# Kernel optimization log

Measured on AMD Instinct MI355X. Metric: run time of the kernel, lower is better.

Reference implementation:

```python
import jax, jax.numpy as jnp
import numpy as np

B, N = 4096, 2048


def setup_inputs() -> dict:
    key = jax.random.key(0)
    k1, k2, k3, k4 = jax.random.split(key, 4)
    return {
        "src_pts3d": jax.random.normal(k1, (B, N, 3), dtype=jnp.float32),
        "tgt_pts3d": jax.random.normal(k2, (B, N, 3), dtype=jnp.float32),
        "kpt_src_mask": jax.random.uniform(k3, (B, N), dtype=jnp.float32),
        "kpt_tgt_mask": jax.random.uniform(k4, (B, N), dtype=jnp.float32),
    }


def reference(src_pts3d, tgt_pts3d, kpt_src_mask, kpt_tgt_mask):
    # H = src^T @ diag(mask_tgt) @ tgt, fused as a masked row-scale contraction: [B,3,3]
    H = jnp.einsum('bnc,bn,bnd->bcd', src_pts3d, kpt_tgt_mask, tgt_pts3d)
    # torch.svd returns V (H = U S V^T); jnp returns Vh, so V = Vh^T
    u, s, vh = jnp.linalg.svd(H)
    v = jnp.swapaxes(vh, -1, -2)              # [B,3,3]
    ut = jnp.swapaxes(u, -1, -2)              # [B,3,3]
    r = v @ ut
    det = jnp.linalg.det(r)                   # [B]
    # branch-free reflection fix: negate 3rd column of V when det(r) < 0
    sign = jnp.where(det < 0, -1.0, 1.0)
    col_scale = jnp.stack([jnp.ones_like(sign), jnp.ones_like(sign), sign], axis=-1)  # [B,3]
    R = (v * col_scale[:, None, :]) @ ut
    return R
```

## Files before the change

### kernel.cpp

```cpp
#include <hip/hip_runtime.h>
#include <math.h>

#define BATCH 4096
#define NPTS  2048
#define THREADS 256

#define ACC(sx, sy, sz, tx, ty, tz, mm) do {                                   \
    float d0 = (mm) * (tx), d1 = (mm) * (ty), d2 = (mm) * (tz);                \
    h[0] = fmaf((sx), d0, h[0]); h[1] = fmaf((sx), d1, h[1]); h[2] = fmaf((sx), d2, h[2]); \
    h[3] = fmaf((sy), d0, h[3]); h[4] = fmaf((sy), d1, h[4]); h[5] = fmaf((sy), d2, h[5]); \
    h[6] = fmaf((sz), d0, h[6]); h[7] = fmaf((sz), d1, h[7]); h[8] = fmaf((sz), d2, h[8]); \
} while (0)

__global__ __launch_bounds__(THREADS)
void reduce_kernel(const float* __restrict__ src, const float* __restrict__ tgt,
                   const float* __restrict__ mask, float* __restrict__ Hout)
{
    const int b = blockIdx.x;
    const float4* s4 = (const float4*)(src  + (size_t)b * (NPTS * 3));
    const float4* t4 = (const float4*)(tgt  + (size_t)b * (NPTS * 3));
    const float4* m4 = (const float4*)(mask + (size_t)b * NPTS);

    float h[9] = {0.f, 0.f, 0.f, 0.f, 0.f, 0.f, 0.f, 0.f, 0.f};

    for (int g = threadIdx.x; g < NPTS / 4; g += THREADS) {
        float4 m  = m4[g];
        float4 sa = s4[3 * g + 0], sb = s4[3 * g + 1], sc = s4[3 * g + 2];
        float4 ta = t4[3 * g + 0], tb = t4[3 * g + 1], tc = t4[3 * g + 2];
        ACC(sa.x, sa.y, sa.z, ta.x, ta.y, ta.z, m.x);
        ACC(sa.w, sb.x, sb.y, ta.w, tb.x, tb.y, m.y);
        ACC(sb.z, sb.w, sc.x, tb.z, tb.w, tc.x, m.z);
        ACC(sc.y, sc.z, sc.w, tc.y, tc.z, tc.w, m.w);
    }

#pragma unroll
    for (int off = 32; off > 0; off >>= 1) {
#pragma unroll
        for (int i = 0; i < 9; ++i) h[i] += __shfl_down(h[i], off);
    }

    __shared__ float sh[THREADS / 64][9];
    const int wid  = threadIdx.x >> 6;
    const int lane = threadIdx.x & 63;
    if (lane == 0) {
#pragma unroll
        for (int i = 0; i < 9; ++i) sh[wid][i] = h[i];
    }
    __syncthreads();

    if (threadIdx.x < 9) {
        const int i = threadIdx.x;
        Hout[(size_t)b * 9 + i] = sh[0][i] + sh[1][i] + sh[2][i] + sh[3][i];
    }
}

__global__ __launch_bounds__(THREADS)
void solve_kernel(const float* __restrict__ Hin, float* __restrict__ out)
{
    const int b = blockIdx.x * THREADS + threadIdx.x;
    if (b >= BATCH) return;

    double H[3][3];
#pragma unroll
    for (int i = 0; i < 9; ++i)
        H[i / 3][i % 3] = (double)Hin[(size_t)b * 9 + i];

    double A[3][3];
#pragma unroll
    for (int i = 0; i < 3; ++i)
#pragma unroll
        for (int j = 0; j < 3; ++j)
            A[i][j] = H[0][i] * H[0][j] + H[1][i] * H[1][j] + H[2][i] * H[2][j];

    double V[3][3] = {{1, 0, 0}, {0, 1, 0}, {0, 0, 1}};

    const int pq[3][3] = {{0, 1, 2}, {0, 2, 1}, {1, 2, 0}};
    for (int sweep = 0; sweep < 6; ++sweep) {
        for (int r = 0; r < 3; ++r) {
            const int p = pq[r][0], q = pq[r][1], k = pq[r][2];
            double apq = A[p][q];
            if (fabs(apq) > 1e-300) {
                double theta = (A[q][q] - A[p][p]) / (2.0 * apq);
                double t = 1.0 / (fabs(theta) + sqrt(theta * theta + 1.0));
                if (theta < 0.0) t = -t;
                double c = 1.0 / sqrt(t * t + 1.0);
                double s = t * c;
                double app = A[p][p], aqq = A[q][q];
                A[p][p] = app - t * apq;
                A[q][q] = aqq + t * apq;
                A[p][q] = A[q][p] = 0.0;
                double akp = A[k][p], akq = A[k][q];
                A[k][p] = A[p][k] = c * akp - s * akq;
                A[k][q] = A[q][k] = s * akp + c * akq;
#pragma unroll
                for (int i = 0; i < 3; ++i) {
                    double vip = V[i][p], viq = V[i][q];
                    V[i][p] = c * vip - s * viq;
                    V[i][q] = s * vip + c * viq;
                }
            }
        }
    }

    int i0 = 0;
    if (A[1][1] > A[i0][i0]) i0 = 1;
    if (A[2][2] > A[i0][i0]) i0 = 2;
    const int ca = (i0 + 1) % 3, cb = (i0 + 2) % 3;
    const int i1 = (A[ca][ca] >= A[cb][cb]) ? ca : cb;

    double v0[3], v1[3];
#pragma unroll
    for (int i = 0; i < 3; ++i) { v0[i] = V[i][i0]; v1[i] = V[i][i1]; }

    double b0[3], b1[3];
#pragma unroll
    for (int r = 0; r < 3; ++r) {
        b0[r] = H[r][0] * v0[0] + H[r][1] * v0[1] + H[r][2] * v0[2];
        b1[r] = H[r][0] * v1[0] + H[r][1] * v1[1] + H[r][2] * v1[2];
    }
    double n0 = b0[0] * b0[0] + b0[1] * b0[1] + b0[2] * b0[2];
    double inv0 = 1.0 / sqrt(fmax(n0, 1e-300));
    double u0[3] = {b0[0] * inv0, b0[1] * inv0, b0[2] * inv0};
    double d01 = u0[0] * b1[0] + u0[1] * b1[1] + u0[2] * b1[2];
    double w[3] = {b1[0] - d01 * u0[0], b1[1] - d01 * u0[1], b1[2] - d01 * u0[2]};
    double nw = w[0] * w[0] + w[1] * w[1] + w[2] * w[2];
    double inv1 = 1.0 / sqrt(fmax(nw, 1e-300));
    double u1[3] = {w[0] * inv1, w[1] * inv1, w[2] * inv1};
    double u2[3] = {u0[1] * u1[2] - u0[2] * u1[1],
                    u0[2] * u1[0] - u0[0] * u1[2],
                    u0[0] * u1[1] - u0[1] * u1[0]};
    double v2[3] = {v0[1] * v1[2] - v0[2] * v1[1],
                    v0[2] * v1[0] - v0[0] * v1[2],
                    v0[0] * v1[1] - v0[1] * v1[0]};

    float* o = out + (size_t)b * 9;
#pragma unroll
    for (int r = 0; r < 3; ++r)
#pragma unroll
        for (int c = 0; c < 3; ++c)
            o[r * 3 + c] = (float)(v0[r] * u0[c] + v1[r] * u1[c] + v2[r] * u2[c]);
}

extern "C" void kernel_launch(void* const* d_in, const int* in_sizes, int n_in,
                              void* d_out, int out_size, void* d_ws, size_t ws_size,
                              hipStream_t stream) {
    const float* src  = (const float*)d_in[0];
    const float* tgt  = (const float*)d_in[1];
    const float* mask = (const float*)d_in[3];
    float* out = (float*)d_out;
    float* Hws = (float*)d_ws;

    reduce_kernel<<<BATCH, THREADS, 0, stream>>>(src, tgt, mask, Hws);
    solve_kernel<<<(BATCH + THREADS - 1) / THREADS, THREADS, 0, stream>>>(Hws, out);
}
```

Baseline: 262.8 us.

## Split each batch reduction across two blocks and combine partials in solve

The reduction grid now launches two blocks per batch item, each handling 1024 points with a single unrolled load per thread instead of a strided loop. The nine partial H sums per block are written to the workspace and added together in double precision inside the solve kernel. The launch bounds also request higher occupancy. The aim is more blocks and more loads in flight, to better saturate HBM bandwidth on a memory-bound reduction. The cost is twice as many block-level reductions and a little extra workspace traffic.

Result: faster. 257.4 us (-2.0%).

```diff
diff --git a/kernel.cpp b/kernel.cpp
--- a/kernel.cpp
+++ b/kernel.cpp
@@ -4,6 +4,9 @@
 #define BATCH 4096
 #define NPTS  2048
 #define THREADS 256
+#define PPB   1024
+#define SUB   (NPTS / PPB)
+#define NBLK  (BATCH * SUB)
 
 #define ACC(sx, sy, sz, tx, ty, tz, mm) do {                                   \
     float d0 = (mm) * (tx), d1 = (mm) * (ty), d2 = (mm) * (tz);                \
@@ -12,26 +15,28 @@
     h[6] = fmaf((sz), d0, h[6]); h[7] = fmaf((sz), d1, h[7]); h[8] = fmaf((sz), d2, h[8]); \
 } while (0)
 
-__global__ __launch_bounds__(THREADS)
+__global__ __launch_bounds__(THREADS, 8)
 void reduce_kernel(const float* __restrict__ src, const float* __restrict__ tgt,
-                   const float* __restrict__ mask, float* __restrict__ Hout)
+                   const float* __restrict__ mask, float* __restrict__ Hpart)
 {
-    const int b = blockIdx.x;
-    const float4* s4 = (const float4*)(src  + (size_t)b * (NPTS * 3));
-    const float4* t4 = (const float4*)(tgt  + (size_t)b * (NPTS * 3));
-    const float4* m4 = (const float4*)(mask + (size_t)b * NPTS);
+    const int blk  = blockIdx.x;
+    const int b    = blk / SUB;
+    const int half = blk % SUB;
+    const int tid  = threadIdx.x;
+
+    const float4* s4 = (const float4*)(src  + (size_t)b * (NPTS * 3) + (size_t)half * (PPB * 3));
+    const float4* t4 = (const float4*)(tgt  + (size_t)b * (NPTS * 3) + (size_t)half * (PPB * 3));
+    const float4* m4 = (const float4*)(mask + (size_t)b * NPTS       + (size_t)half * PPB);
+
+    float4 m  = m4[tid];
+    float4 sa = s4[3 * tid], sb = s4[3 * tid + 1], sc = s4[3 * tid + 2];
+    float4 ta = t4[3 * tid], tb = t4[3 * tid + 1], tc = t4[3 * tid + 2];
 
     float h[9] = {0.f, 0.f, 0.f, 0.f, 0.f, 0.f, 0.f, 0.f, 0.f};
-
-    for (int g = threadIdx.x; g < NPTS / 4; g += THREADS) {
-        float4 m  = m4[g];
-        float4 sa = s4[3 * g + 0], sb = s4[3 * g + 1], sc = s4[3 * g + 2];
-        float4 ta = t4[3 * g + 0], tb = t4[3 * g + 1], tc = t4[3 * g + 2];
-        ACC(sa.x, sa.y, sa.z, ta.x, ta.y, ta.z, m.x);
-        ACC(sa.w, sb.x, sb.y, ta.w, tb.x, tb.y, m.y);
-        ACC(sb.z, sb.w, sc.x, tb.z, tb.w, tc.x, m.z);
-        ACC(sc.y, sc.z, sc.w, tc.y, tc.z, tc.w, m.w);
-    }
+    ACC(sa.x, sa.y, sa.z, ta.x, ta.y, ta.z, m.x);
+    ACC(sa.w, sb.x, sb.y, ta.w, tb.x, tb.y, m.y);
+    ACC(sb.z, sb.w, sc.x, tb.z, tb.w, tc.x, m.z);
+    ACC(sc.y, sc.z, sc.w, tc.y, tc.z, tc.w, m.w);
 
 #pragma unroll
     for (int off = 32; off > 0; off >>= 1) {
@@ -39,31 +44,36 @@
         for (int i = 0; i < 9; ++i) h[i] += __shfl_down(h[i], off);
     }
 
-    __shared__ float sh[THREADS / 64][9];
-    const int wid  = threadIdx.x >> 6;
-    const int lane = threadIdx.x & 63;
+    __shared__ float shred[THREADS / 64][9];
+    const int wid  = tid >> 6;
+    const int lane = tid & 63;
     if (lane == 0) {
 #pragma unroll
-        for (int i = 0; i < 9; ++i) sh[wid][i] = h[i];
+        for (int i = 0; i < 9; ++i) shred[wid][i] = h[i];
     }
     __syncthreads();
 
-    if (threadIdx.x < 9) {
-        const int i = threadIdx.x;
-        Hout[(size_t)b * 9 + i] = sh[0][i] + sh[1][i] + sh[2][i] + sh[3][i];
+    if (tid < 9) {
+        Hpart[(size_t)blk * 9 + tid] =
+            shred[0][tid] + shred[1][tid] + shred[2][tid] + shred[3][tid];
     }
 }
 
 __global__ __launch_bounds__(THREADS)
-void solve_kernel(const float* __restrict__ Hin, float* __restrict__ out)
+void solve_kernel(const float* __restrict__ Hpart, float* __restrict__ out)
 {
     const int b = blockIdx.x * THREADS + threadIdx.x;
     if (b >= BATCH) return;
 
     double H[3][3];
 #pragma unroll
-    for (int i = 0; i < 9; ++i)
-        H[i / 3][i % 3] = (double)Hin[(size_t)b * 9 + i];
+    for (int i = 0; i < 9; ++i) {
+        double v = 0.0;
+#pragma unroll
+        for (int s = 0; s < SUB; ++s)
+            v += (double)Hpart[((size_t)b * SUB + s) * 9 + i];
+        H[i / 3][i % 3] = v;
+    }
 
     double A[3][3];
 #pragma unroll
@@ -150,6 +160,6 @@
     float* out = (float*)d_out;
     float* Hws = (float*)d_ws;
 
-    reduce_kernel<<<BATCH, THREADS, 0, stream>>>(src, tgt, mask, Hws);
+    reduce_kernel<<<NBLK, THREADS, 0, stream>>>(src, tgt, mask, Hws);
     solve_kernel<<<(BATCH + THREADS - 1) / THREADS, THREADS, 0, stream>>>(Hws, out);
 }
```
